# Optimization experiments

Measured on AMD Instinct MI355X. Metric: run time of the kernel, lower is better.

## Reference

```python
import jax, jax.numpy as jnp
import numpy as np

B, L, D = 2, 4096, 1024      # batch, seq_len, d_model (expand_ratio=1 -> d_inner == D)
DS, RK, K = 16, 64, 3        # d_state, dt_rank, conv kernel size
EPS = 1e-5


def setup_inputs() -> dict:
    key = jax.random.key(0)
    ks = jax.random.split(key, 16)
    s = 0.02
    inp = {
        "x":      jax.random.normal(ks[0], (B, L, D), jnp.float32),
        "gamma":  jnp.ones((D,), jnp.float32),
        "beta":   jnp.zeros((D,), jnp.float32),
        "W_in":   jax.random.normal(ks[1], (D, 2 * D), jnp.float32) * s,
        "conv_w": jax.random.normal(ks[2], (K, 1, D), jnp.float32) * s,   # depthwise (k, 1, d)
        "conv_b": jnp.zeros((D,), jnp.float32),
        "W_xp":   jax.random.normal(ks[3], (D, RK), jnp.float32) * s,
        "W_Bg":   jax.random.normal(ks[4], (D, DS), jnp.float32) * s,
        "W_Cg":   jax.random.normal(ks[5], (D, DS), jnp.float32) * s,
        "W_dt":   jax.random.normal(ks[6], (RK, D), jnp.float32) * s,
        "b_dt":   jnp.zeros((D,), jnp.float32),
        "W_Bp":   jax.random.normal(ks[7], (DS, D), jnp.float32) * s,
        "W_Cp":   jax.random.normal(ks[8], (DS, D), jnp.float32) * s,
        "A":      -jnp.exp(jax.random.normal(ks[9], (D,), jnp.float32) * 0.5),  # negative for stability
        "D_skip": jnp.ones((D,), jnp.float32),
        "W_out":  jax.random.normal(ks[10], (D, D), jnp.float32) * s,
    }
    return inp


def reference(x, gamma, beta, W_in, conv_w, conv_b, W_xp, W_Bg, W_Cg,
              W_dt, b_dt, W_Bp, W_Cp, A, D_skip, W_out):
    d = x.shape[-1]
    # 1. LayerNorm
    mu = jnp.mean(x, -1, keepdims=True)
    var = jnp.mean(jnp.square(x - mu), -1, keepdims=True)
    xn = (x - mu) * jax.lax.rsqrt(var + EPS) * gamma + beta
    # 2. in_proj + split into main/gate branch
    xz = xn @ W_in                                 # (b, l, 2d)
    xb, z = jnp.split(xz, 2, axis=-1)
    # 3. depthwise Conv1D (same padding) + SiLU
    xc = jax.lax.conv_general_dilated(
        xb, conv_w, window_strides=(1,), padding='SAME',
        dimension_numbers=('NWC', 'WIO', 'NWC'), feature_group_count=d) + conv_b
    x_act = jax.nn.silu(xc)                        # (b, l, d)
    # SSM parameter generation
    delta = jax.nn.softplus((x_act @ W_xp) @ W_dt + b_dt)   # (b, l, d)
    Bm = (x_act @ W_Bg) @ W_Bp                     # (b, l, d)
    Cm = (x_act @ W_Cg) @ W_Cp                     # (b, l, d)
    # 4. diagonal selective scan: h_t = exp(delta*A)*h_{t-1} + delta*B*x ; y = C*h
    dA = jnp.exp(delta * A)
    dBx = delta * Bm * x_act
    def step(h, ab):
        a, bx = ab
        h = a * h + bx
        return h, h
    h0 = jnp.zeros_like(dA[:, 0])
    _, hs = jax.lax.scan(step, h0, (dA.transpose(1, 0, 2), dBx.transpose(1, 0, 2)))
    y = Cm * hs.transpose(1, 0, 2)
    # 5. skip-D, gating, out_proj + residual
    out_ssm = y + x_act * D_skip
    gated = out_ssm * jax.nn.silu(z)
    return gated @ W_out + x
```

## Files before the change

kernel.cpp:

```cpp
#include <hip/hip_runtime.h>
#include <math.h>

#define BB 2
#define LL 4096
#define DD 1024
#define DS 16
#define RK 64
#define MM (BB*LL)
#define NC 128
#define LC (LL/NC)

typedef __attribute__((ext_vector_type(8))) short short8;
typedef __attribute__((ext_vector_type(4))) float f32x4;

__device__ __forceinline__ unsigned short f2bf(float f) {
    union { float f; unsigned u; } v; v.f = f;
    unsigned r = v.u + 0x7fff + ((v.u >> 16) & 1);
    return (unsigned short)(r >> 16);
}
__device__ __forceinline__ float bf2f(unsigned short u) {
    union { unsigned u; float f; } v; v.u = ((unsigned)u) << 16;
    return v.f;
}
__device__ __forceinline__ float2 bf2x2(unsigned u) {
    return make_float2(bf2f((unsigned short)u), bf2f((unsigned short)(u >> 16)));
}
__device__ __forceinline__ unsigned f2bfx2(float lo, float hi) {
    return (unsigned)f2bf(lo) | ((unsigned)f2bf(hi) << 16);
}
__device__ __forceinline__ float fast_rcp(float x) {
    return __builtin_amdgcn_rcpf(x);
}
__device__ __forceinline__ float silu_f(float v) {
    return v * fast_rcp(1.0f + __expf(-v));
}
__device__ __forceinline__ void gload16(const void* g, void* l) {
    __builtin_amdgcn_global_load_lds(
        (const __attribute__((address_space(1))) unsigned int*)g,
        (__attribute__((address_space(3))) unsigned int*)l, 16, 0, 0);
}

__global__ __launch_bounds__(256)
void ln_kernel(const float* __restrict__ x, const float* __restrict__ gamma,
               const float* __restrict__ beta, unsigned short* __restrict__ xn_bf) {
    int row = blockIdx.x;
    int tid = threadIdx.x;
    const float4* xr = (const float4*)(x + (size_t)row * DD);
    float4 v = xr[tid];
    float s = v.x + v.y + v.z + v.w;
    float q = v.x*v.x + v.y*v.y + v.z*v.z + v.w*v.w;
    #pragma unroll
    for (int off = 32; off > 0; off >>= 1) {
        s += __shfl_down(s, off);
        q += __shfl_down(q, off);
    }
    __shared__ float ss[4], qq[4];
    int wv = tid >> 6;
    if ((tid & 63) == 0) { ss[wv] = s; qq[wv] = q; }
    __syncthreads();
    float S = ss[0] + ss[1] + ss[2] + ss[3];
    float Q = qq[0] + qq[1] + qq[2] + qq[3];
    float mu  = S * (1.0f / DD);
    float var = Q * (1.0f / DD) - mu * mu;
    float r = rsqrtf(var + 1e-5f);
    int d0 = tid * 4;
    float4 gv = *(const float4*)(gamma + d0);
    float4 bv = *(const float4*)(beta + d0);
    ushort4 o;
    o.x = f2bf((v.x - mu) * r * gv.x + bv.x);
    o.y = f2bf((v.y - mu) * r * gv.y + bv.y);
    o.z = f2bf((v.z - mu) * r * gv.z + bv.z);
    o.w = f2bf((v.w - mu) * r * gv.w + bv.w);
    *(ushort4*)&xn_bf[(size_t)row * DD + d0] = o;
}

__global__ __launch_bounds__(256)
void transpose_bf16(const float* __restrict__ W, unsigned short* __restrict__ WT,
                    int K, int N) {
    __shared__ float t[32][33];
    int n0 = blockIdx.x * 32, k0 = blockIdx.y * 32;
    int tx = threadIdx.x & 31, ty = threadIdx.x >> 5;
    #pragma unroll
    for (int r = 0; r < 32; r += 8)
        t[ty + r][tx] = W[(size_t)(k0 + ty + r) * N + n0 + tx];
    __syncthreads();
    #pragma unroll
    for (int r = 0; r < 32; r += 8) {
        int nl = ty + r;
        WT[(size_t)(n0 + nl) * K + k0 + tx] = f2bf(t[tx][nl]);
    }
}

__global__ __launch_bounds__(256)
void build_wg(const float* __restrict__ W_xp, const float* __restrict__ W_Bg,
              const float* __restrict__ W_Cg, unsigned short* __restrict__ WgT) {
    int idx = blockIdx.x * 256 + threadIdx.x;
    int k = idx & 1023, n = idx >> 10;
    float v = 0.0f;
    if (n < 64)       v = W_xp[k * RK + n];
    else if (n < 80)  v = W_Bg[k * DS + (n - 64)];
    else if (n < 96)  v = W_Cg[k * DS + (n - 80)];
    WgT[idx] = f2bf(v);
}

__global__ __launch_bounds__(256)
void build_wup(const float* __restrict__ W_dt, const float* __restrict__ W_Bp,
               const float* __restrict__ W_Cp, unsigned short* __restrict__ WupT) {
    int idx = blockIdx.x * 256 + threadIdx.x;
    int k = idx & 127, n = idx >> 7;
    float v = 0.0f;
    if (n < 1024)      { if (k < 64)            v = W_dt[k * 1024 + n]; }
    else if (n < 2048) { if (k >= 64 && k < 80) v = W_Bp[(k - 64) * 1024 + (n - 1024)]; }
    else               { if (k >= 80 && k < 96) v = W_Cp[(k - 80) * 1024 + (n - 2048)]; }
    WupT[idx] = f2bf(v);
}

#define MF(a, b, c) __builtin_amdgcn_mfma_f32_16x16x32_bf16(a, b, c, 0, 0, 0)
template<int EPI>
__global__ __launch_bounds__(512, 1)
void gemm256(const unsigned short* __restrict__ A, const unsigned short* __restrict__ BT,
             void* __restrict__ C0v, void* __restrict__ C1v,
             const float* __restrict__ res, int M, int N, int K) {
    extern __shared__ unsigned short sm[];
    unsigned short* As = sm;
    unsigned short* Bs = sm + 32768;
    const int tid = threadIdx.x;
    const int wave = tid >> 6, lane = tid & 63;
    const int wr = wave >> 2, wc = wave & 3;
    const int fr = lane & 15, fs = lane >> 4;

    int nbx = gridDim.x;
    int nwg = nbx * gridDim.y;
    int bid = blockIdx.y * nbx + blockIdx.x;
    int cpx = nwg >> 3;
    int swz = (bid & 7) * cpx + (bid >> 3);
    int by = swz / nbx, bx = swz - by * nbx;
    size_t rb = (size_t)by * 256, cb = (size_t)bx * 256;

    const int srow = tid >> 3;
    const int ssw  = (tid & 7) ^ (srow & 7);
    const unsigned short* gA = A + (rb + srow) * K + ssw * 8;
    const unsigned short* gB = BT + (cb + srow) * K + ssw * 8;
    const size_t rstep = (size_t)64 * K;
    unsigned short* dA = As + tid * 8;
    unsigned short* dB = Bs + tid * 8;
    const int T = K >> 6;

#define STG(rnd, buf, kt) do { \
    gload16(gA + (size_t)(rnd) * rstep + (size_t)(kt) * 64, dA + (buf) * 16384 + (rnd) * 4096); \
    gload16(gB + (size_t)(rnd) * rstep + (size_t)(kt) * 64, dB + (buf) * 16384 + (rnd) * 4096); } while (0)
#define FOFF(r, S) (((r) << 6) + ((((S) ^ ((r) & 7))) << 3))
#define LDA(i, kk) (*(const short8*)&Ab[FOFF(arow0 + ((i) << 4), fs + ((kk) << 2))])
#define LDB(j, kk) (*(const short8*)&Bb[FOFF(brow0 + ((j) << 4), fs + ((kk) << 2))])

    const int arow0 = wr * 128 + fr;
    const int brow0 = wc * 64 + fr;

    f32x4 acc[8][4] = {};

    STG(0, 0, 0); STG(1, 0, 0); STG(2, 0, 0); STG(3, 0, 0);

    #pragma unroll 1
    for (int t = 0; t < T; ++t) {
        const int cur = t & 1, nx = cur ^ 1;
        const bool pf = (t + 1) < T;
        const unsigned short* Ab = As + cur * 16384;
        const unsigned short* Bb = Bs + cur * 16384;

        if (pf) { STG(0, nx, t + 1); }
        if (pf) { asm volatile("s_waitcnt vmcnt(2)" ::: "memory"); }
        else    { asm volatile("s_waitcnt vmcnt(0)" ::: "memory"); }
        __builtin_amdgcn_s_barrier();
        __builtin_amdgcn_sched_barrier(0);

        short8 bfr[4][2];
        #pragma unroll
        for (int j = 0; j < 4; ++j) {
            bfr[j][0] = LDB(j, 0);
            bfr[j][1] = LDB(j, 1);
        }
        __builtin_amdgcn_s_setprio(1);
        #pragma unroll
        for (int ii = 0; ii < 2; ++ii) {
            short8 a0 = LDA(ii, 0), a1 = LDA(ii, 1);
            #pragma unroll
            for (int j = 0; j < 4; ++j) {
                acc[ii][j] = MF(a0, bfr[j][0], acc[ii][j]);
                acc[ii][j] = MF(a1, bfr[j][1], acc[ii][j]);
            }
        }
        __builtin_amdgcn_s_setprio(0);
        __builtin_amdgcn_sched_barrier(0);

        #pragma unroll
        for (int p = 1; p < 4; ++p) {
            if (pf) { STG(p, nx, t + 1); }
            __builtin_amdgcn_s_setprio(1);
            #pragma unroll
            for (int ii = 0; ii < 2; ++ii) {
                const int i = 2 * p + ii;
                short8 a0 = LDA(i, 0), a1 = LDA(i, 1);
                #pragma unroll
                for (int j = 0; j < 4; ++j) {
                    acc[i][j] = MF(a0, bfr[j][0], acc[i][j]);
                    acc[i][j] = MF(a1, bfr[j][1], acc[i][j]);
                }
            }
            __builtin_amdgcn_s_setprio(0);
            __builtin_amdgcn_sched_barrier(0);
        }
        __builtin_amdgcn_s_barrier();
    }

    const int row0 = (int)rb + wr * 128 + fs * 4;
    const int col0 = (int)cb + wc * 64 + fr;
    if (EPI == 1) {
        unsigned short* Cd = (cb < DD) ? (unsigned short*)C0v : (unsigned short*)C1v;
        const int cadj = (cb < DD) ? 0 : -DD;
        #pragma unroll
        for (int i = 0; i < 8; ++i)
            #pragma unroll
            for (int j = 0; j < 4; ++j) {
                int col = col0 + cadj + (j << 4);
                #pragma unroll
                for (int q = 0; q < 4; ++q)
                    Cd[(size_t)(row0 + (i << 4) + q) * DD + col] = f2bf(acc[i][j][q]);
            }
    } else {
        float* C0 = (float*)C0v;
        #pragma unroll
        for (int i = 0; i < 8; ++i)
            #pragma unroll
            for (int j = 0; j < 4; ++j) {
                int col = col0 + (j << 4);
                #pragma unroll
                for (int q = 0; q < 4; ++q) {
                    size_t off = (size_t)(row0 + (i << 4) + q) * N + col;
                    C0[off] = acc[i][j][q] + res[off];
                }
            }
    }
#undef STG
#undef FOFF
#undef LDA
#undef LDB
}

template<int EPI>
__global__ __launch_bounds__(256)
void gemm_mfma(const unsigned short* __restrict__ A, const unsigned short* __restrict__ BT,
               void* __restrict__ C0v, void* __restrict__ C1v,
               const float* __restrict__ res, int M, int N, int K) {
    __shared__ unsigned short As[128 * 32];
    __shared__ unsigned short Bs[128 * 32];
    int tid = threadIdx.x;
    int rb = blockIdx.y * 128, cb = blockIdx.x * 128;
    int wave = tid >> 6, lane = tid & 63;
    int wr = wave >> 1, wc = wave & 1;
    int fr = lane & 15, fs = lane >> 4;

    int r0 = tid >> 2, s0 = tid & 3;
    int sw0 = s0 ^ ((r0 >> 1) & 3);
    const unsigned short* gA = A + (size_t)(rb + r0) * K + sw0 * 8;
    const unsigned short* gB = BT + (size_t)(cb + r0) * K + sw0 * 8;
    size_t half = (size_t)64 * K;
    char* lA0 = (char*)As + tid * 16;
    char* lA1 = (char*)As + (tid + 256) * 16;
    char* lB0 = (char*)Bs + tid * 16;
    char* lB1 = (char*)Bs + (tid + 256) * 16;

    int kb = 0, ke = K;
    if (EPI == 3) { kb = blockIdx.z * (K >> 2); ke = kb + (K >> 2); }

    f32x4 acc[4][4] = {};

    #pragma unroll 1
    for (int k0 = kb; k0 < ke; k0 += 32) {
        __syncthreads();
        gload16(gA + k0, lA0);
        gload16(gA + half + k0, lA1);
        gload16(gB + k0, lB0);
        gload16(gB + half + k0, lB1);
        __syncthreads();

        short8 af[4], bfr[4];
        #pragma unroll
        for (int i = 0; i < 4; i++) {
            int row = (wr << 6) + (i << 4) + fr;
            int off = (row << 5) + ((fs ^ ((row >> 1) & 3)) << 3);
            af[i] = *(const short8*)&As[off];
        }
        #pragma unroll
        for (int j = 0; j < 4; j++) {
            int row = (wc << 6) + (j << 4) + fr;
            int off = (row << 5) + ((fs ^ ((row >> 1) & 3)) << 3);
            bfr[j] = *(const short8*)&Bs[off];
        }
        #pragma unroll
        for (int i = 0; i < 4; i++)
            #pragma unroll
            for (int j = 0; j < 4; j++)
                acc[i][j] = MF(af[i], bfr[j], acc[i][j]);
    }

    int row0 = rb + (wr << 6) + (fs << 2);
    int col0 = (wc << 6) + fr;
    if (EPI == 0) {
        unsigned short* C0 = (unsigned short*)C0v;
        #pragma unroll
        for (int i = 0; i < 4; i++)
            #pragma unroll
            for (int j = 0; j < 4; j++) {
                int col = cb + col0 + (j << 4);
                #pragma unroll
                for (int q = 0; q < 4; q++)
                    C0[(size_t)(row0 + (i << 4) + q) * N + col] = f2bf(acc[i][j][q]);
            }
    } else if (EPI == 4) {
        unsigned short* C0 = (unsigned short*)C0v;
        const bool isdelta = (cb < DD);
        #pragma unroll
        for (int i = 0; i < 4; i++)
            #pragma unroll
            for (int j = 0; j < 4; j++) {
                int col = cb + col0 + (j << 4);
                float bias = isdelta ? res[col] : 0.0f;
                #pragma unroll
                for (int q = 0; q < 4; q++) {
                    float v = acc[i][j][q];
                    if (isdelta) {
                        v += bias;
                        v = fmaxf(v, 0.0f) + __logf(1.0f + __expf(-fabsf(v)));
                    }
                    C0[(size_t)(row0 + (i << 4) + q) * N + col] = f2bf(v);
                }
            }
    } else {
        float* C0 = (float*)C0v + (size_t)blockIdx.z * M * N;
        #pragma unroll
        for (int i = 0; i < 4; i++)
            #pragma unroll
            for (int j = 0; j < 4; j++) {
                int col = cb + col0 + (j << 4);
                #pragma unroll
                for (int q = 0; q < 4; q++)
                    C0[(size_t)(row0 + (i << 4) + q) * N + col] = acc[i][j][q];
            }
    }
}

__global__ __launch_bounds__(256)
void reduce_t(const float* __restrict__ tp, unsigned short* __restrict__ t_bf) {
    int idx = blockIdx.x * 256 + threadIdx.x;
    const size_t Q = (size_t)MM * 128 / 4;
    float4 a = ((const float4*)tp)[idx];
    float4 b = ((const float4*)tp)[idx + Q];
    float4 c = ((const float4*)tp)[idx + 2 * Q];
    float4 d = ((const float4*)tp)[idx + 3 * Q];
    ushort4 o;
    o.x = f2bf(a.x + b.x + c.x + d.x);
    o.y = f2bf(a.y + b.y + c.y + d.y);
    o.z = f2bf(a.z + b.z + c.z + d.z);
    o.w = f2bf(a.w + b.w + c.w + d.w);
    ((ushort4*)t_bf)[idx] = o;
}

__global__ __launch_bounds__(256)
void conv_silu(const unsigned short* __restrict__ xb, const float* __restrict__ cw,
               const float* __restrict__ cb, unsigned short* __restrict__ xact) {
    int idx8 = blockIdx.x * 256 + threadIdx.x;
    size_t e = (size_t)idx8 * 8;
    int d0 = (int)(e & (DD - 1));
    int bl = (int)(e >> 10);
    int l = bl & (LL - 1);
    short8 cur = *(const short8*)&xb[e];
    short8 prv = {}, nxt = {};
    if (l > 0)      prv = *(const short8*)&xb[e - DD];
    if (l < LL - 1) nxt = *(const short8*)&xb[e + DD];
    short8 o;
    #pragma unroll
    for (int j = 0; j < 8; j++) {
        int d = d0 + j;
        float acc = cb[d];
        acc = fmaf(bf2f((unsigned short)prv[j]), cw[0 * DD + d], acc);
        acc = fmaf(bf2f((unsigned short)cur[j]), cw[1 * DD + d], acc);
        acc = fmaf(bf2f((unsigned short)nxt[j]), cw[2 * DD + d], acc);
        o[j] = (short)f2bf(silu_f(acc));
    }
    *(short8*)&xact[e] = o;
}

__global__ __launch_bounds__(256)
void scan_p1(const unsigned short* __restrict__ dbc, const unsigned short* __restrict__ xact,
             const float* __restrict__ A, float* __restrict__ P, float* __restrict__ Hc) {
    int d = (blockIdx.x * 256 + threadIdx.x) * 2;
    int c = blockIdx.y, b = blockIdx.z;
    float2 a_d = *(const float2*)&A[d];
    size_t row0 = (size_t)(b * LL + c * LC);
    float h0 = 0.0f, h1 = 0.0f, sd0 = 0.0f, sd1 = 0.0f;
    #pragma unroll 4
    for (int i = 0; i < LC; i++) {
        size_t r = row0 + i;
        const unsigned short* pd = &dbc[r * 3072 + d];
        float2 dl = bf2x2(*(const unsigned*)pd);
        float2 bm = bf2x2(*(const unsigned*)(pd + 1024));
        float2 xa = bf2x2(*(const unsigned*)&xact[r * DD + d]);
        float a0 = __expf(dl.x * a_d.x);
        float a1 = __expf(dl.y * a_d.y);
        h0 = fmaf(a0, h0, dl.x * bm.x * xa.x);
        h1 = fmaf(a1, h1, dl.y * bm.y * xa.y);
        sd0 += dl.x; sd1 += dl.y;
    }
    int pc = (b * NC + c) * DD + d;
    *(float2*)&P[pc]  = make_float2(__expf(a_d.x * sd0), __expf(a_d.y * sd1));
    *(float2*)&Hc[pc] = make_float2(h0, h1);
}

__global__ __launch_bounds__(256)
void scan_p2(const float* __restrict__ P, const float* __restrict__ Hc,
             float* __restrict__ hin) {
    int d = blockIdx.x * 256 + threadIdx.x;
    int b = blockIdx.y;
    float carry = 0.0f;
    for (int c = 0; c < NC; c++) {
        int o = (b * NC + c) * DD + d;
        hin[o] = carry;
        carry = fmaf(P[o], carry, Hc[o]);
    }
}

__global__ __launch_bounds__(256)
void scan_p3(const unsigned short* __restrict__ dbc, const unsigned short* __restrict__ xact,
             const unsigned short* __restrict__ zb, const float* __restrict__ hin,
             const float* __restrict__ A, const float* __restrict__ Dsk,
             unsigned short* __restrict__ g) {
    int d = (blockIdx.x * 256 + threadIdx.x) * 2;
    int c = blockIdx.y, b = blockIdx.z;
    float2 a_d = *(const float2*)&A[d];
    float2 dsk = *(const float2*)&Dsk[d];
    float2 hv = *(const float2*)&hin[(b * NC + c) * DD + d];
    float h0 = hv.x, h1 = hv.y;
    size_t row0 = (size_t)(b * LL + c * LC);
    #pragma unroll 4
    for (int i = 0; i < LC; i++) {
        size_t r = row0 + i;
        const unsigned short* pd = &dbc[r * 3072 + d];
        float2 dl = bf2x2(*(const unsigned*)pd);
        float2 bm = bf2x2(*(const unsigned*)(pd + 1024));
        float2 cm = bf2x2(*(const unsigned*)(pd + 2048));
        size_t o = r * DD + d;
        float2 xa = bf2x2(*(const unsigned*)&xact[o]);
        float2 zv = bf2x2(*(const unsigned*)&zb[o]);
        float a0 = __expf(dl.x * a_d.x);
        float a1 = __expf(dl.y * a_d.y);
        h0 = fmaf(a0, h0, dl.x * bm.x * xa.x);
        h1 = fmaf(a1, h1, dl.y * bm.y * xa.y);
        float os0 = fmaf(xa.x, dsk.x, cm.x * h0);
        float os1 = fmaf(xa.y, dsk.y, cm.y * h1);
        float g0 = os0 * silu_f(zv.x);
        float g1 = os1 * silu_f(zv.y);
        *(unsigned*)&g[o] = f2bfx2(g0, g1);
    }
}

extern "C" void kernel_launch(void* const* d_in, const int* in_sizes, int n_in,
                              void* d_out, int out_size, void* d_ws, size_t ws_size,
                              hipStream_t stream) {
    const float* x      = (const float*)d_in[0];
    const float* gamma  = (const float*)d_in[1];
    const float* beta   = (const float*)d_in[2];
    const float* W_in   = (const float*)d_in[3];
    const float* conv_w = (const float*)d_in[4];
    const float* conv_b = (const float*)d_in[5];
    const float* W_xp   = (const float*)d_in[6];
    const float* W_Bg   = (const float*)d_in[7];
    const float* W_Cg   = (const float*)d_in[8];
    const float* W_dt   = (const float*)d_in[9];
    const float* b_dt   = (const float*)d_in[10];
    const float* W_Bp   = (const float*)d_in[11];
    const float* W_Cp   = (const float*)d_in[12];
    const float* A      = (const float*)d_in[13];
    const float* Dsk    = (const float*)d_in[14];
    const float* W_out  = (const float*)d_in[15];
    float* out = (float*)d_out;

    const size_t BIG = (size_t)MM * DD;
    char* p = (char*)d_ws;
    unsigned short* xn_bf  = (unsigned short*)p;  p += BIG * 2;
    unsigned short* xb_bf  = (unsigned short*)p;  p += BIG * 2;
    unsigned short* z_bf   = (unsigned short*)p;  p += BIG * 2;
    unsigned short* xact_bf= (unsigned short*)p;  p += BIG * 2;
    unsigned short* t_bf   = (unsigned short*)p;  p += (size_t)MM * 128 * 2;
    unsigned short* dBC    = (unsigned short*)p;  p += (size_t)MM * 3072 * 2;
    float* tpart = (float*)p;                     p += (size_t)4 * MM * 128 * 4;
    float* P     = (float*)p;                     p += (size_t)BB * NC * DD * 4;
    float* Hc    = (float*)p;                     p += (size_t)BB * NC * DD * 4;
    float* hin   = (float*)p;                     p += (size_t)BB * NC * DD * 4;
    unsigned short* WinT  = (unsigned short*)p;   p += (size_t)2 * DD * DD * 2;
    unsigned short* WoutT = (unsigned short*)p;   p += (size_t)DD * DD * 2;
    unsigned short* WgT   = (unsigned short*)p;   p += (size_t)128 * DD * 2;
    unsigned short* WupT  = (unsigned short*)p;   p += (size_t)3072 * 128 * 2;
    unsigned short* g_bf  = xn_bf;

    {
        void (*k1)(const unsigned short*, const unsigned short*, void*, void*,
                   const float*, int, int, int) = gemm256<1>;
        void (*k2)(const unsigned short*, const unsigned short*, void*, void*,
                   const float*, int, int, int) = gemm256<2>;
        (void)hipFuncSetAttribute((const void*)k1,
            hipFuncAttributeMaxDynamicSharedMemorySize, 131072);
        (void)hipFuncSetAttribute((const void*)k2,
            hipFuncAttributeMaxDynamicSharedMemorySize, 131072);
    }

    transpose_bf16<<<dim3(2 * DD / 32, DD / 32), 256, 0, stream>>>(W_in, WinT, DD, 2 * DD);
    transpose_bf16<<<dim3(DD / 32, DD / 32), 256, 0, stream>>>(W_out, WoutT, DD, DD);
    build_wg<<<(128 * DD) / 256, 256, 0, stream>>>(W_xp, W_Bg, W_Cg, WgT);
    build_wup<<<(3072 * 128) / 256, 256, 0, stream>>>(W_dt, W_Bp, W_Cp, WupT);
    ln_kernel<<<MM, 256, 0, stream>>>(x, gamma, beta, xn_bf);
    gemm256<1><<<dim3(2 * DD / 256, MM / 256), 512, 131072, stream>>>(
        xn_bf, WinT, xb_bf, z_bf, nullptr, MM, 2 * DD, DD);
    conv_silu<<<(MM * DD / 8) / 256, 256, 0, stream>>>(xb_bf, conv_w, conv_b, xact_bf);
    gemm_mfma<3><<<dim3(1, MM / 128, 4), 256, 0, stream>>>(
        xact_bf, WgT, tpart, nullptr, nullptr, MM, 128, DD);
    reduce_t<<<(MM * 128 / 4) / 256, 256, 0, stream>>>(tpart, t_bf);
    gemm_mfma<4><<<dim3(3072 / 128, MM / 128), 256, 0, stream>>>(
        t_bf, WupT, dBC, nullptr, b_dt, MM, 3072, 128);
    scan_p1<<<dim3(DD / 512, NC, BB), 256, 0, stream>>>(dBC, xact_bf, A, P, Hc);
    scan_p2<<<dim3(DD / 256, BB), 256, 0, stream>>>(P, Hc, hin);
    scan_p3<<<dim3(DD / 512, NC, BB), 256, 0, stream>>>(dBC, xact_bf, z_bf, hin,
                                                        A, Dsk, g_bf);
    gemm256<2><<<dim3(DD / 256, MM / 256), 512, 131072, stream>>>(
        g_bf, WoutT, out, nullptr, x, MM, DD, DD);
}
```

Measured before the change: 185.0 us.

## Retune big GEMM schedule, specialize small GEMMs, bf16 partials, more scan chunks

Several changes land together. The 256-tile GEMM main loop now issues LDS loads for A fragments ahead of the MFMA phases, with explicit barriers and lgkmcnt waits so that loads and compute interleave across waves. The low-rank up-projection GEMM gets a dedicated kernel that loads the whole K=128 slab into swizzled LDS at once instead of looping over 32-wide K steps. Split-K partials of the down-projection are stored in bf16 rather than fp32, halving that traffic at some cost in accuracy. The scan chunk count doubles to 256 for more parallelism in the chunked scan phases, and the carry loop is unrolled.

```diff
diff --git a/kernel.cpp b/kernel.cpp
--- a/kernel.cpp
+++ b/kernel.cpp
@@ -7,7 +7,7 @@
 #define DS 16
 #define RK 64
 #define MM (BB*LL)
-#define NC 128
+#define NC 256
 #define LC (LL/NC)
 
 typedef __attribute__((ext_vector_type(8))) short short8;
@@ -179,37 +179,52 @@
             bfr[j][0] = LDB(j, 0);
             bfr[j][1] = LDB(j, 1);
         }
-        __builtin_amdgcn_s_setprio(1);
-        #pragma unroll
-        for (int ii = 0; ii < 2; ++ii) {
-            short8 a0 = LDA(ii, 0), a1 = LDA(ii, 1);
+        {
+            short8 a00 = LDA(0, 0), a01 = LDA(0, 1);
+            short8 a10 = LDA(1, 0), a11 = LDA(1, 1);
+            __builtin_amdgcn_s_barrier();
+            asm volatile("s_waitcnt lgkmcnt(0)" ::: "memory");
+            __builtin_amdgcn_sched_barrier(0);
+            __builtin_amdgcn_s_setprio(1);
             #pragma unroll
             for (int j = 0; j < 4; ++j) {
-                acc[ii][j] = MF(a0, bfr[j][0], acc[ii][j]);
-                acc[ii][j] = MF(a1, bfr[j][1], acc[ii][j]);
-            }
-        }
-        __builtin_amdgcn_s_setprio(0);
-        __builtin_amdgcn_sched_barrier(0);
-
-        #pragma unroll
-        for (int p = 1; p < 4; ++p) {
-            if (pf) { STG(p, nx, t + 1); }
-            __builtin_amdgcn_s_setprio(1);
-            #pragma unroll
-            for (int ii = 0; ii < 2; ++ii) {
-                const int i = 2 * p + ii;
-                short8 a0 = LDA(i, 0), a1 = LDA(i, 1);
-                #pragma unroll
-                for (int j = 0; j < 4; ++j) {
-                    acc[i][j] = MF(a0, bfr[j][0], acc[i][j]);
-                    acc[i][j] = MF(a1, bfr[j][1], acc[i][j]);
-                }
+                acc[0][j] = MF(a00, bfr[j][0], acc[0][j]);
+                acc[1][j] = MF(a10, bfr[j][0], acc[1][j]);
+            }
+            #pragma unroll
+            for (int j = 0; j < 4; ++j) {
+                acc[0][j] = MF(a01, bfr[j][1], acc[0][j]);
+                acc[1][j] = MF(a11, bfr[j][1], acc[1][j]);
             }
             __builtin_amdgcn_s_setprio(0);
             __builtin_amdgcn_sched_barrier(0);
-        }
-        __builtin_amdgcn_s_barrier();
+            __builtin_amdgcn_s_barrier();
+        }
+
+        #pragma unroll
+        for (int p = 1; p < 4; ++p) {
+            const int i0 = 2 * p;
+            short8 a00 = LDA(i0, 0),     a01 = LDA(i0, 1);
+            short8 a10 = LDA(i0 + 1, 0), a11 = LDA(i0 + 1, 1);
+            if (pf) { STG(p, nx, t + 1); }
+            __builtin_amdgcn_s_barrier();
+            asm volatile("s_waitcnt lgkmcnt(0)" ::: "memory");
+            __builtin_amdgcn_sched_barrier(0);
+            __builtin_amdgcn_s_setprio(1);
+            #pragma unroll
+            for (int j = 0; j < 4; ++j) {
+                acc[i0][j]     = MF(a00, bfr[j][0], acc[i0][j]);
+                acc[i0 + 1][j] = MF(a10, bfr[j][0], acc[i0 + 1][j]);
+            }
+            #pragma unroll
+            for (int j = 0; j < 4; ++j) {
+                acc[i0][j]     = MF(a01, bfr[j][1], acc[i0][j]);
+                acc[i0 + 1][j] = MF(a11, bfr[j][1], acc[i0 + 1][j]);
+            }
+            __builtin_amdgcn_s_setprio(0);
+            __builtin_amdgcn_sched_barrier(0);
+            __builtin_amdgcn_s_barrier();
+        }
     }
 
     const int row0 = (int)rb + wr * 128 + fs * 4;
@@ -246,11 +261,75 @@
 #undef LDB
 }
 
-template<int EPI>
-__global__ __launch_bounds__(256)
-void gemm_mfma(const unsigned short* __restrict__ A, const unsigned short* __restrict__ BT,
-               void* __restrict__ C0v, void* __restrict__ C1v,
-               const float* __restrict__ res, int M, int N, int K) {
+__global__ __launch_bounds__(256)
+void gemm_up(const unsigned short* __restrict__ A, const unsigned short* __restrict__ BT,
+             unsigned short* __restrict__ C, const float* __restrict__ bias, int N) {
+    __shared__ unsigned short As[128 * 128];
+    __shared__ unsigned short Bs[128 * 128];
+    int tid = threadIdx.x;
+    int rb = blockIdx.y * 128, cb = blockIdx.x * 128;
+    int wave = tid >> 6, lane = tid & 63;
+    int wr = wave >> 1, wc = wave & 1;
+    int fr = lane & 15, fs = lane >> 4;
+
+    int srow16 = tid >> 4, sseg = tid & 15;
+    #pragma unroll
+    for (int r = 0; r < 8; ++r) {
+        int row = r * 16 + srow16;
+        int ss = sseg ^ (row & 15);
+        gload16(A + (size_t)(rb + row) * 128 + ss * 8, (char*)As + r * 4096 + tid * 16);
+        gload16(BT + (size_t)(cb + row) * 128 + ss * 8, (char*)Bs + r * 4096 + tid * 16);
+    }
+    asm volatile("s_waitcnt vmcnt(0)" ::: "memory");
+    __syncthreads();
+
+    f32x4 acc[4][4] = {};
+    #pragma unroll
+    for (int kk = 0; kk < 4; ++kk) {
+        short8 af[4], bfr[4];
+        #pragma unroll
+        for (int i = 0; i < 4; ++i) {
+            int row = (wr << 6) + (i << 4) + fr;
+            int s = (fs + (kk << 2)) ^ (row & 15);
+            af[i] = *(const short8*)&As[row * 128 + s * 8];
+        }
+        #pragma unroll
+        for (int j = 0; j < 4; ++j) {
+            int row = (wc << 6) + (j << 4) + fr;
+            int s = (fs + (kk << 2)) ^ (row & 15);
+            bfr[j] = *(const short8*)&Bs[row * 128 + s * 8];
+        }
+        #pragma unroll
+        for (int i = 0; i < 4; ++i)
+            #pragma unroll
+            for (int j = 0; j < 4; ++j)
+                acc[i][j] = MF(af[i], bfr[j], acc[i][j]);
+    }
+
+    int row0 = rb + (wr << 6) + (fs << 2);
+    int col0 = (wc << 6) + fr;
+    const bool isdelta = (cb < DD);
+    #pragma unroll
+    for (int i = 0; i < 4; ++i)
+        #pragma unroll
+        for (int j = 0; j < 4; ++j) {
+            int col = cb + col0 + (j << 4);
+            float bv = isdelta ? bias[col] : 0.0f;
+            #pragma unroll
+            for (int q = 0; q < 4; ++q) {
+                float v = acc[i][j][q];
+                if (isdelta) {
+                    v += bv;
+                    v = fmaxf(v, 0.0f) + __logf(1.0f + __expf(-fabsf(v)));
+                }
+                C[(size_t)(row0 + (i << 4) + q) * N + col] = f2bf(v);
+            }
+        }
+}
+
+__global__ __launch_bounds__(256)
+void gemm_down(const unsigned short* __restrict__ A, const unsigned short* __restrict__ BT,
+               unsigned short* __restrict__ C0, int M, int N, int K) {
     __shared__ unsigned short As[128 * 32];
     __shared__ unsigned short Bs[128 * 32];
     int tid = threadIdx.x;
@@ -269,8 +348,7 @@
     char* lB0 = (char*)Bs + tid * 16;
     char* lB1 = (char*)Bs + (tid + 256) * 16;
 
-    int kb = 0, ke = K;
-    if (EPI == 3) { kb = blockIdx.z * (K >> 2); ke = kb + (K >> 2); }
+    int kb = blockIdx.z * (K >> 2), ke = kb + (K >> 2);
 
     f32x4 acc[4][4] = {};
 
@@ -305,63 +383,31 @@
 
     int row0 = rb + (wr << 6) + (fs << 2);
     int col0 = (wc << 6) + fr;
-    if (EPI == 0) {
-        unsigned short* C0 = (unsigned short*)C0v;
-        #pragma unroll
-        for (int i = 0; i < 4; i++)
-            #pragma unroll
-            for (int j = 0; j < 4; j++) {
-                int col = cb + col0 + (j << 4);
-                #pragma unroll
-                for (int q = 0; q < 4; q++)
-                    C0[(size_t)(row0 + (i << 4) + q) * N + col] = f2bf(acc[i][j][q]);
-            }
-    } else if (EPI == 4) {
-        unsigned short* C0 = (unsigned short*)C0v;
-        const bool isdelta = (cb < DD);
-        #pragma unroll
-        for (int i = 0; i < 4; i++)
-            #pragma unroll
-            for (int j = 0; j < 4; j++) {
-                int col = cb + col0 + (j << 4);
-                float bias = isdelta ? res[col] : 0.0f;
-                #pragma unroll
-                for (int q = 0; q < 4; q++) {
-                    float v = acc[i][j][q];
-                    if (isdelta) {
-                        v += bias;
-                        v = fmaxf(v, 0.0f) + __logf(1.0f + __expf(-fabsf(v)));
-                    }
-                    C0[(size_t)(row0 + (i << 4) + q) * N + col] = f2bf(v);
-                }
-            }
-    } else {
-        float* C0 = (float*)C0v + (size_t)blockIdx.z * M * N;
-        #pragma unroll
-        for (int i = 0; i < 4; i++)
-            #pragma unroll
-            for (int j = 0; j < 4; j++) {
-                int col = cb + col0 + (j << 4);
-                #pragma unroll
-                for (int q = 0; q < 4; q++)
-                    C0[(size_t)(row0 + (i << 4) + q) * N + col] = acc[i][j][q];
-            }
-    }
-}
-
-__global__ __launch_bounds__(256)
-void reduce_t(const float* __restrict__ tp, unsigned short* __restrict__ t_bf) {
+    unsigned short* Cp = C0 + (size_t)blockIdx.z * M * N;
+    #pragma unroll
+    for (int i = 0; i < 4; i++)
+        #pragma unroll
+        for (int j = 0; j < 4; j++) {
+            int col = cb + col0 + (j << 4);
+            #pragma unroll
+            for (int q = 0; q < 4; q++)
+                Cp[(size_t)(row0 + (i << 4) + q) * N + col] = f2bf(acc[i][j][q]);
+        }
+}
+
+__global__ __launch_bounds__(256)
+void reduce_t(const unsigned short* __restrict__ tp, unsigned short* __restrict__ t_bf) {
     int idx = blockIdx.x * 256 + threadIdx.x;
-    const size_t Q = (size_t)MM * 128 / 4;
-    float4 a = ((const float4*)tp)[idx];
-    float4 b = ((const float4*)tp)[idx + Q];
-    float4 c = ((const float4*)tp)[idx + 2 * Q];
-    float4 d = ((const float4*)tp)[idx + 3 * Q];
+    const size_t Q = (size_t)MM * 128;
+    ushort4 a = ((const ushort4*)tp)[idx];
+    ushort4 b = ((const ushort4*)(tp + Q))[idx];
+    ushort4 c = ((const ushort4*)(tp + 2 * Q))[idx];
+    ushort4 d = ((const ushort4*)(tp + 3 * Q))[idx];
     ushort4 o;
-    o.x = f2bf(a.x + b.x + c.x + d.x);
-    o.y = f2bf(a.y + b.y + c.y + d.y);
-    o.z = f2bf(a.z + b.z + c.z + d.z);
-    o.w = f2bf(a.w + b.w + c.w + d.w);
+    o.x = f2bf(bf2f(a.x) + bf2f(b.x) + bf2f(c.x) + bf2f(d.x));
+    o.y = f2bf(bf2f(a.y) + bf2f(b.y) + bf2f(c.y) + bf2f(d.y));
+    o.z = f2bf(bf2f(a.z) + bf2f(b.z) + bf2f(c.z) + bf2f(d.z));
+    o.w = f2bf(bf2f(a.w) + bf2f(b.w) + bf2f(c.w) + bf2f(d.w));
     ((ushort4*)t_bf)[idx] = o;
 }
 
@@ -422,6 +468,7 @@
     int d = blockIdx.x * 256 + threadIdx.x;
     int b = blockIdx.y;
     float carry = 0.0f;
+    #pragma unroll 4
     for (int c = 0; c < NC; c++) {
         int o = (b * NC + c) * DD + d;
         hin[o] = carry;
@@ -492,7 +539,7 @@
     unsigned short* xact_bf= (unsigned short*)p;  p += BIG * 2;
     unsigned short* t_bf   = (unsigned short*)p;  p += (size_t)MM * 128 * 2;
     unsigned short* dBC    = (unsigned short*)p;  p += (size_t)MM * 3072 * 2;
-    float* tpart = (float*)p;                     p += (size_t)4 * MM * 128 * 4;
+    unsigned short* tpart  = (unsigned short*)p;  p += (size_t)4 * MM * 128 * 2;
     float* P     = (float*)p;                     p += (size_t)BB * NC * DD * 4;
     float* Hc    = (float*)p;                     p += (size_t)BB * NC * DD * 4;
     float* hin   = (float*)p;                     p += (size_t)BB * NC * DD * 4;
@@ -521,11 +568,11 @@
     gemm256<1><<<dim3(2 * DD / 256, MM / 256), 512, 131072, stream>>>(
         xn_bf, WinT, xb_bf, z_bf, nullptr, MM, 2 * DD, DD);
     conv_silu<<<(MM * DD / 8) / 256, 256, 0, stream>>>(xb_bf, conv_w, conv_b, xact_bf);
-    gemm_mfma<3><<<dim3(1, MM / 128, 4), 256, 0, stream>>>(
-        xact_bf, WgT, tpart, nullptr, nullptr, MM, 128, DD);
+    gemm_down<<<dim3(1, MM / 128, 4), 256, 0, stream>>>(
+        xact_bf, WgT, tpart, MM, 128, DD);
     reduce_t<<<(MM * 128 / 4) / 256, 256, 0, stream>>>(tpart, t_bf);
-    gemm_mfma<4><<<dim3(3072 / 128, MM / 128), 256, 0, stream>>>(
-        t_bf, WupT, dBC, nullptr, b_dt, MM, 3072, 128);
+    gemm_up<<<dim3(3072 / 128, MM / 128), 256, 0, stream>>>(
+        t_bf, WupT, dBC, b_dt, 3072);
     scan_p1<<<dim3(DD / 512, NC, BB), 256, 0, stream>>>(dBC, xact_bf, A, P, Hc);
     scan_p2<<<dim3(DD / 256, BB), 256, 0, stream>>>(P, Hc, hin);
     scan_p3<<<dim3(DD / 512, NC, BB), 256, 0, stream>>>(dBC, xact_bf, z_bf, hin,
```

Measured after the change: 218.6 us. 1.18x slower.
